# Kernel optimization log

Hardware: AMD Instinct MI355X
Metric: run time of the kernel (lower is better)

## Reference

```python
import jax, jax.numpy as jnp
import numpy as np

N_NODES = 50000
N_EDGES = 800000
D_FEAT = 64      # input_size
D_OUT = 64       # output_size
N_REL = 8
N_BASES = 4


def setup_inputs() -> dict:
    key = jax.random.key(0)
    k1, k2, k3, k4, k5, k6 = jax.random.split(key, 6)
    x = jax.random.normal(k1, (N_NODES, D_FEAT, N_REL), dtype=jnp.float32)
    edge_src = jax.random.randint(k2, (N_EDGES,), 0, N_NODES, dtype=jnp.int32)
    edge_dst = jax.random.randint(k3, (N_EDGES,), 0, N_NODES, dtype=jnp.int32)
    edge_weight = jax.random.uniform(k4, (N_EDGES,), dtype=jnp.float32)
    # basis-decomposed relation weights (xavier-like scale)
    w_bases = jax.random.normal(k5, (N_BASES, D_FEAT, D_OUT), dtype=jnp.float32) * (2.0 / (D_FEAT + D_OUT)) ** 0.5
    w_rel = jax.random.normal(k6, (N_REL, N_BASES), dtype=jnp.float32) * (2.0 / (N_REL + N_BASES)) ** 0.5
    return {"x": x, "edge_src": edge_src, "edge_dst": edge_dst,
            "edge_weight": edge_weight, "w_bases": w_bases, "w_rel": w_rel}


def reference(x, edge_src, edge_dst, edge_weight, w_bases, w_rel):
    # w[r] = sum_b w_rel[r,b] * w_bases[b]  -> [R, d_in, d_out]
    w = jnp.einsum('rb,bio->rio', w_rel, w_bases)
    n_rel = x.shape[-1]
    n_nodes = x.shape[0]
    # sparse adjacency message passing per relation: support_r = A @ x[:, :, r]
    # A @ y == segment_sum over edges (dst <- weight * y[src])
    supports = []
    for r in range(n_rel):  # small fixed relation count
        msgs = edge_weight[:, None] * x[edge_src, :, r]          # [E, d_in]
        agg = jax.ops.segment_sum(msgs, edge_dst, num_segments=n_nodes)  # [N, d_in]
        supports.append(agg)
    tmp = jnp.concatenate(supports, axis=1)                      # [N, R*d_in]
    weights = w.reshape(n_rel * x.shape[1], w.shape[2])          # [R*d_in, d_out]
    out = tmp @ weights                                          # [N, d_out]
    return out
```

## Files before the change

kernel.cpp:

```cpp
#include <hip/hip_runtime.h>
#include <hip/hip_bf16.h>

#define DFEAT   64
#define NREL    8
#define KDIM    512
#define DOUT    64
#define NBASES  4

typedef short short8 __attribute__((ext_vector_type(8)));
typedef float f32x4  __attribute__((ext_vector_type(4)));
typedef unsigned short ushort8 __attribute__((ext_vector_type(8)));

__device__ __forceinline__ unsigned short f2bf(float f) {
    unsigned u = __float_as_uint(f);
    u += 0x7fff + ((u >> 16) & 1);
    return (unsigned short)(u >> 16);
}
__device__ __forceinline__ float bf2f(unsigned short b) {
    return __uint_as_float(((unsigned)b) << 16);
}

__global__ __launch_bounds__(256) void weight_kernel(
    const float* __restrict__ w_rel,
    const float* __restrict__ w_bases,
    unsigned short* __restrict__ wT,
    int* __restrict__ cnt, int n_nodes)
{
    int idx = blockIdx.x * 256 + threadIdx.x;
    int k = idx & 511;
    int o = idx >> 9;
    int i = k >> 3;
    int r = k & 7;
    float s = 0.f;
#pragma unroll
    for (int b = 0; b < NBASES; ++b)
        s += w_rel[r * NBASES + b] * w_bases[(b * DFEAT + i) * DOUT + o];
    wT[o * KDIM + k] = f2bf(s);

    for (int j = idx; j < n_nodes; j += KDIM * DOUT)
        cnt[j] = 0;
}

__global__ __launch_bounds__(256) void fused_kernel(
    const float* __restrict__ x,
    const unsigned short* __restrict__ wT,
    unsigned short* __restrict__ y,
    int n_nodes,
    const int* __restrict__ esrc, const int* __restrict__ edst,
    const float* __restrict__ ew,
    int* __restrict__ cnt, unsigned* __restrict__ bucket,
    int n_edges, int cap, int t_blocks)
{
    const int tid = threadIdx.x;

    if (blockIdx.x >= t_blocks) {
        int e = (blockIdx.x - t_blocks) * 256 + tid;
        if (e < n_edges) {
            int d = edst[e];
            int pos = atomicAdd(&cnt[d], 1);
            if (pos < cap) {
                bucket[(size_t)d * cap + pos] =
                    (unsigned)(esrc[e] & 0xFFFF) | ((unsigned)f2bf(ew[e]) << 16);
            }
        }
        return;
    }

    __shared__ unsigned short ylds[4][16][64];

    const int wid  = tid >> 6;
    const int lane = tid & 63;
    const int quad = lane >> 4;
    const int fi   = lane & 15;

    const int node0 = (blockIdx.x * 4 + wid) * 16;
    int myrow = node0 + fi;
    if (myrow >= n_nodes) myrow = n_nodes - 1;
    const float* xg = x + (size_t)myrow * KDIM + quad * 8;
    const unsigned short* wg = wT + fi * KDIM + quad * 8;

    f32x4 acc0 = {0.f, 0.f, 0.f, 0.f};
    f32x4 acc1 = {0.f, 0.f, 0.f, 0.f};
    f32x4 acc2 = {0.f, 0.f, 0.f, 0.f};
    f32x4 acc3 = {0.f, 0.f, 0.f, 0.f};

#pragma unroll 4
    for (int kb = 0; kb < KDIM; kb += 32) {
        float4 xa = *(const float4*)(xg + kb);
        float4 xb = *(const float4*)(xg + kb + 4);
        short8 a;
        a[0] = f2bf(xa.x); a[1] = f2bf(xa.y); a[2] = f2bf(xa.z); a[3] = f2bf(xa.w);
        a[4] = f2bf(xb.x); a[5] = f2bf(xb.y); a[6] = f2bf(xb.z); a[7] = f2bf(xb.w);

        short8 b0 = *(const short8*)(wg + kb);
        short8 b1 = *(const short8*)(wg + 16 * KDIM + kb);
        short8 b2 = *(const short8*)(wg + 32 * KDIM + kb);
        short8 b3 = *(const short8*)(wg + 48 * KDIM + kb);

        acc0 = __builtin_amdgcn_mfma_f32_16x16x32_bf16(a, b0, acc0, 0, 0, 0);
        acc1 = __builtin_amdgcn_mfma_f32_16x16x32_bf16(a, b1, acc1, 0, 0, 0);
        acc2 = __builtin_amdgcn_mfma_f32_16x16x32_bf16(a, b2, acc2, 0, 0, 0);
        acc3 = __builtin_amdgcn_mfma_f32_16x16x32_bf16(a, b3, acc3, 0, 0, 0);
    }

#pragma unroll
    for (int r = 0; r < 4; ++r) {
        int n = quad * 4 + r;
        ylds[wid][n][fi]      = f2bf(acc0[r]);
        ylds[wid][n][16 + fi] = f2bf(acc1[r]);
        ylds[wid][n][32 + fi] = f2bf(acc2[r]);
        ylds[wid][n][48 + fi] = f2bf(acc3[r]);
    }
    __syncthreads();

    int nl = lane >> 2;
    int cg = (lane & 3) * 16;
    int node = node0 + nl;
    if (node < n_nodes) {
        ushort8 v0 = *(const ushort8*)&ylds[wid][nl][cg];
        ushort8 v1 = *(const ushort8*)&ylds[wid][nl][cg + 8];
        unsigned short* yr = y + (size_t)node * DOUT + cg;
        *(ushort8*)yr       = v0;
        *(ushort8*)(yr + 8) = v1;
    }
}

__global__ __launch_bounds__(256) void gather_kernel(
    const int* __restrict__ cnt, const unsigned* __restrict__ bucket,
    const unsigned short* __restrict__ y,
    float* __restrict__ out, int n_nodes, int cap)
{
    int node = blockIdx.x * 4 + (threadIdx.x >> 6);
    int lane = threadIdx.x & 63;
    int sub = lane >> 3;
    int fi  = lane & 7;
    if (node >= n_nodes) return;

    int deg = cnt[node];
    if (deg > cap) deg = cap;

    unsigned entry = 0;
    if (lane < deg) entry = bucket[(size_t)node * cap + lane];

    float acc[8];
#pragma unroll
    for (int j = 0; j < 8; ++j) acc[j] = 0.f;

    for (int c = 0; c < deg; c += 16) {
        unsigned p0 = __shfl((int)entry, c + sub);
        unsigned p1 = __shfl((int)entry, c + 8 + sub);
        float w0 = __uint_as_float(p0 & 0xFFFF0000u);
        float w1 = __uint_as_float(p1 & 0xFFFF0000u);
        ushort8 y0 = *(const ushort8*)(y + (size_t)(p0 & 0xFFFFu) * DOUT + fi * 8);
        ushort8 y1 = *(const ushort8*)(y + (size_t)(p1 & 0xFFFFu) * DOUT + fi * 8);
#pragma unroll
        for (int j = 0; j < 8; ++j) {
            acc[j] += w0 * bf2f(y0[j]);
            acc[j] += w1 * bf2f(y1[j]);
        }
    }

#pragma unroll
    for (int mask = 8; mask <= 32; mask <<= 1)
#pragma unroll
        for (int j = 0; j < 8; ++j)
            acc[j] += __shfl_xor(acc[j], mask);

    if (sub == 0) {
        float* orow = out + (size_t)node * DOUT + fi * 8;
        *(float4*)orow       = make_float4(acc[0], acc[1], acc[2], acc[3]);
        *(float4*)(orow + 4) = make_float4(acc[4], acc[5], acc[6], acc[7]);
    }
}

extern "C" void kernel_launch(void* const* d_in, const int* in_sizes, int n_in,
                              void* d_out, int out_size, void* d_ws, size_t ws_size,
                              hipStream_t stream) {
    const float* x       = (const float*)d_in[0];
    const int*   esrc    = (const int*)d_in[1];
    const int*   edst    = (const int*)d_in[2];
    const float* ew      = (const float*)d_in[3];
    const float* w_bases = (const float*)d_in[4];
    const float* w_rel   = (const float*)d_in[5];
    float* out = (float*)d_out;

    const int n_nodes = in_sizes[0] / KDIM;
    const int n_edges = in_sizes[1];

    size_t base_words = (size_t)n_nodes * 32 + 16384 + n_nodes;
    int cap = 64;
    while (cap > 16 && (base_words + (size_t)n_nodes * cap) * 4 > ws_size)
        cap -= 16;

    unsigned short* y   = (unsigned short*)d_ws;
    unsigned short* wT  = y + (size_t)n_nodes * DOUT;
    int*      cnt       = (int*)(wT + KDIM * DOUT);
    unsigned* bucket    = (unsigned*)(cnt + n_nodes);

    weight_kernel<<<(KDIM * DOUT) / 256, 256, 0, stream>>>(
        w_rel, w_bases, wT, cnt, n_nodes);

    const int t_blocks = (n_nodes + 63) / 64;
    const int p_blocks = (n_edges + 255) / 256;
    fused_kernel<<<t_blocks + p_blocks, 256, 0, stream>>>(
        x, wT, y, n_nodes,
        esrc, edst, ew, cnt, bucket, n_edges, cap, t_blocks);

    int gblocks = (n_nodes + 3) / 4;
    gather_kernel<<<gblocks, 256, 0, stream>>>(cnt, bucket, y, out, n_nodes, cap);
}
```

Measured before the change: 230.4 us.

## Two-level binning of edges by destination chunk before bucket scatter

Edge placement changes from one global atomic per edge into a per-node bucket to a two-stage scheme. Each block first bins 2048 edges into shared memory by destination chunk and appends them to per-chunk slabs. A new scatter kernel then places each chunk's records using shared-memory counters over a node sub-range. The aim is to localize the random global atomics and bucket writes so they hit L2/MCs with better locality, and the gather is reordered chunk-major to match. The cost is an extra kernel launch, slab traffic, and each scatter block rereading its whole chunk slab (SB-fold redundant reads).

```diff
diff --git a/kernel.cpp b/kernel.cpp
--- a/kernel.cpp
+++ b/kernel.cpp
@@ -7,6 +7,11 @@
 #define DOUT    64
 #define NBASES  4
 
+#define NCHUNK  8
+#define EPB     2048
+#define CAPB    352
+#define SB      8
+
 typedef short short8 __attribute__((ext_vector_type(8)));
 typedef float f32x4  __attribute__((ext_vector_type(4)));
 typedef unsigned short ushort8 __attribute__((ext_vector_type(8)));
@@ -24,7 +29,7 @@
     const float* __restrict__ w_rel,
     const float* __restrict__ w_bases,
     unsigned short* __restrict__ wT,
-    int* __restrict__ cnt, int n_nodes)
+    int* __restrict__ cnt, int* __restrict__ cursor, int n_nodes)
 {
     int idx = blockIdx.x * 256 + threadIdx.x;
     int k = idx & 511;
@@ -37,9 +42,20 @@
         s += w_rel[r * NBASES + b] * w_bases[(b * DFEAT + i) * DOUT + o];
     wT[o * KDIM + k] = f2bf(s);
 
+    if (idx < 16) cursor[idx] = 0;
     for (int j = idx; j < n_nodes; j += KDIM * DOUT)
         cnt[j] = 0;
 }
+
+union SharedK2 {
+    unsigned short ylds[4][16][64];
+    struct {
+        uint2 bin[NCHUNK][CAPB];
+        int bcnt[NCHUNK];
+        int bful[NCHUNK];
+        int bbase[NCHUNK];
+    } b;
+};
 
 __global__ __launch_bounds__(256) void fused_kernel(
     const float* __restrict__ x,
@@ -48,25 +64,61 @@
     int n_nodes,
     const int* __restrict__ esrc, const int* __restrict__ edst,
     const float* __restrict__ ew,
-    int* __restrict__ cnt, unsigned* __restrict__ bucket,
-    int n_edges, int cap, int t_blocks)
+    int* __restrict__ cnt, int* __restrict__ cursor,
+    unsigned* __restrict__ bucket, uint2* __restrict__ slab,
+    int n_edges, int cap, int slab_cap, int chsz, int t_blocks)
 {
     const int tid = threadIdx.x;
+    __shared__ SharedK2 sh;
 
     if (blockIdx.x >= t_blocks) {
-        int e = (blockIdx.x - t_blocks) * 256 + tid;
-        if (e < n_edges) {
-            int d = edst[e];
-            int pos = atomicAdd(&cnt[d], 1);
-            if (pos < cap) {
-                bucket[(size_t)d * cap + pos] =
-                    (unsigned)(esrc[e] & 0xFFFF) | ((unsigned)f2bf(ew[e]) << 16);
+        auto& B = sh.b;
+        if (tid < NCHUNK) B.bcnt[tid] = 0;
+        __syncthreads();
+
+        int e0 = (blockIdx.x - t_blocks) * EPB + tid;
+#pragma unroll
+        for (int j = 0; j < EPB / 256; ++j) {
+            int e = e0 + j * 256;
+            if (e < n_edges) {
+                int d = edst[e];
+                unsigned entry = (unsigned)(esrc[e] & 0xFFFF)
+                               | ((unsigned)f2bf(ew[e]) << 16);
+                int c = d / chsz;
+                int pos = atomicAdd(&B.bcnt[c], 1);
+                if (pos < CAPB) {
+                    B.bin[c][pos] = make_uint2(entry, (unsigned)d);
+                } else {
+                    int p = atomicAdd(&cnt[d], 1);
+                    if (p < cap) bucket[(size_t)d * cap + p] = entry;
+                }
             }
         }
+        __syncthreads();
+
+        if (tid < NCHUNK) {
+            int n = B.bcnt[tid]; if (n > CAPB) n = CAPB;
+            B.bful[tid] = n;
+            B.bbase[tid] = atomicAdd(&cursor[tid], n);
+        }
+        __syncthreads();
+
+#pragma unroll 1
+        for (int c = 0; c < NCHUNK; ++c) {
+            int n = B.bful[c], bb = B.bbase[c];
+            uint2* sc = slab + (size_t)c * slab_cap;
+            for (int i = tid; i < n; i += 256) {
+                uint2 rec = B.bin[c][i];
+                if (bb + i < slab_cap) {
+                    sc[bb + i] = rec;
+                } else {
+                    int p = atomicAdd(&cnt[(int)rec.y], 1);
+                    if (p < cap) bucket[(size_t)rec.y * cap + p] = rec.x;
+                }
+            }
+        }
         return;
     }
-
-    __shared__ unsigned short ylds[4][16][64];
 
     const int wid  = tid >> 6;
     const int lane = tid & 63;
@@ -106,10 +158,10 @@
 #pragma unroll
     for (int r = 0; r < 4; ++r) {
         int n = quad * 4 + r;
-        ylds[wid][n][fi]      = f2bf(acc0[r]);
-        ylds[wid][n][16 + fi] = f2bf(acc1[r]);
-        ylds[wid][n][32 + fi] = f2bf(acc2[r]);
-        ylds[wid][n][48 + fi] = f2bf(acc3[r]);
+        sh.ylds[wid][n][fi]      = f2bf(acc0[r]);
+        sh.ylds[wid][n][16 + fi] = f2bf(acc1[r]);
+        sh.ylds[wid][n][32 + fi] = f2bf(acc2[r]);
+        sh.ylds[wid][n][48 + fi] = f2bf(acc3[r]);
     }
     __syncthreads();
 
@@ -117,38 +169,74 @@
     int cg = (lane & 3) * 16;
     int node = node0 + nl;
     if (node < n_nodes) {
-        ushort8 v0 = *(const ushort8*)&ylds[wid][nl][cg];
-        ushort8 v1 = *(const ushort8*)&ylds[wid][nl][cg + 8];
+        ushort8 v0 = *(const ushort8*)&sh.ylds[wid][nl][cg];
+        ushort8 v1 = *(const ushort8*)&sh.ylds[wid][nl][cg + 8];
         unsigned short* yr = y + (size_t)node * DOUT + cg;
         *(ushort8*)yr       = v0;
         *(ushort8*)(yr + 8) = v1;
     }
 }
 
+__global__ __launch_bounds__(1024) void scatter_kernel(
+    const uint2* __restrict__ slab, const int* __restrict__ cursor,
+    int* __restrict__ cnt, unsigned* __restrict__ bucket,
+    int n_nodes, int cap, int chsz, int slab_cap)
+{
+    __shared__ int lcnt[1024];
+    const int tid = threadIdx.x;
+    const int c = blockIdx.x & (NCHUNK - 1);
+    const int s = blockIdx.x / NCHUNK;
+    const int srsz  = (chsz + SB - 1) / SB;
+    const int nbase = c * chsz + s * srsz;
+    int nspan = srsz;
+    if (nspan > chsz - s * srsz)  nspan = chsz - s * srsz;
+    if (nspan > n_nodes - nbase)  nspan = n_nodes - nbase;
+    if (nspan < 0) nspan = 0;
+
+    for (int i = tid; i < nspan; i += 1024) lcnt[i] = cnt[nbase + i];
+    __syncthreads();
+
+    int total = cursor[c]; if (total > slab_cap) total = slab_cap;
+    const uint2* sl = slab + (size_t)c * slab_cap;
+    for (int i = tid; i < total; i += 1024) {
+        uint2 rec = sl[i];
+        int rel = (int)rec.y - nbase;
+        if ((unsigned)rel < (unsigned)nspan) {
+            int pos = atomicAdd(&lcnt[rel], 1);
+            if (pos < cap)
+                bucket[(size_t)rec.y * cap + pos] = rec.x;
+        }
+    }
+    __syncthreads();
+    for (int i = tid; i < nspan; i += 1024) cnt[nbase + i] = lcnt[i];
+}
+
 __global__ __launch_bounds__(256) void gather_kernel(
     const int* __restrict__ cnt, const unsigned* __restrict__ bucket,
     const unsigned short* __restrict__ y,
-    float* __restrict__ out, int n_nodes, int cap)
+    float* __restrict__ out, int n_nodes, int cap, int chsz)
 {
-    int node = blockIdx.x * 4 + (threadIdx.x >> 6);
+    const int c = blockIdx.x & (NCHUNK - 1);
+    const int q = blockIdx.x / NCHUNK;
+    int rel  = q * 4 + (threadIdx.x >> 6);
+    int node = c * chsz + rel;
     int lane = threadIdx.x & 63;
     int sub = lane >> 3;
     int fi  = lane & 7;
-    if (node >= n_nodes) return;
+    if (rel >= chsz || node >= n_nodes) return;
 
     int deg = cnt[node];
+    unsigned entry = (lane < cap) ? bucket[(size_t)node * cap + lane] : 0u;
     if (deg > cap) deg = cap;
-
-    unsigned entry = 0;
-    if (lane < deg) entry = bucket[(size_t)node * cap + lane];
+    if (lane >= deg) entry = 0;
 
     float acc[8];
 #pragma unroll
     for (int j = 0; j < 8; ++j) acc[j] = 0.f;
 
-    for (int c = 0; c < deg; c += 16) {
-        unsigned p0 = __shfl((int)entry, c + sub);
-        unsigned p1 = __shfl((int)entry, c + 8 + sub);
+    for (int cc = 0; cc < deg; cc += 16) {
+        unsigned p0 = __shfl((int)entry, cc + sub);
+        unsigned p1 = __shfl((int)entry, cc + 8 + sub);
         float w0 = __uint_as_float(p0 & 0xFFFF0000u);
         float w1 = __uint_as_float(p1 & 0xFFFF0000u);
         ushort8 y0 = *(const ushort8*)(y + (size_t)(p0 & 0xFFFFu) * DOUT + fi * 8);
@@ -186,26 +274,39 @@
 
     const int n_nodes = in_sizes[0] / KDIM;
     const int n_edges = in_sizes[1];
-
-    size_t base_words = (size_t)n_nodes * 32 + 16384 + n_nodes;
+    const int chsz = (n_nodes + NCHUNK - 1) / NCHUNK;
+
+    size_t wsw = ws_size / 4;
+    size_t base_words = (size_t)n_nodes * 32 + 16384 + n_nodes + 16;
     int cap = 64;
-    while (cap > 16 && (base_words + (size_t)n_nodes * cap) * 4 > ws_size)
+    while (cap > 16 && base_words + (size_t)n_nodes * cap > wsw)
         cap -= 16;
+    size_t used = base_words + (size_t)n_nodes * cap;
+    size_t rem = (wsw > used) ? (wsw - used) : 0;
+    size_t sc = rem / 16;
+    int slab_cap = (int)(sc > 131072 ? 131072 : sc);
 
     unsigned short* y   = (unsigned short*)d_ws;
     unsigned short* wT  = y + (size_t)n_nodes * DOUT;
     int*      cnt       = (int*)(wT + KDIM * DOUT);
-    unsigned* bucket    = (unsigned*)(cnt + n_nodes);
+    int*      cursor    = cnt + n_nodes;
+    unsigned* bucket    = (unsigned*)(cursor + 16);
+    uint2*    slab      = (uint2*)(bucket + (size_t)n_nodes * cap);
 
     weight_kernel<<<(KDIM * DOUT) / 256, 256, 0, stream>>>(
-        w_rel, w_bases, wT, cnt, n_nodes);
+        w_rel, w_bases, wT, cnt, cursor, n_nodes);
 
     const int t_blocks = (n_nodes + 63) / 64;
-    const int p_blocks = (n_edges + 255) / 256;
+    const int p_blocks = (n_edges + EPB - 1) / EPB;
     fused_kernel<<<t_blocks + p_blocks, 256, 0, stream>>>(
         x, wT, y, n_nodes,
-        esrc, edst, ew, cnt, bucket, n_edges, cap, t_blocks);
-
-    int gblocks = (n_nodes + 3) / 4;
-    gather_kernel<<<gblocks, 256, 0, stream>>>(cnt, bucket, y, out, n_nodes, cap);
-}
+        esrc, edst, ew, cnt, cursor, bucket, slab,
+        n_edges, cap, slab_cap, chsz, t_blocks);
+
+    scatter_kernel<<<NCHUNK * SB, 1024, 0, stream>>>(
+        slab, cursor, cnt, bucket, n_nodes, cap, chsz, slab_cap);
+
+    const int gblocks = NCHUNK * ((chsz + 3) / 4);
+    gather_kernel<<<gblocks, 256, 0, stream>>>(
+        cnt, bucket, y, out, n_nodes, cap, chsz);
+}
```

Result: slower. 246.7 us (+7.1%).

## Replace per-node buckets with coarse chunk binning and LDS-atomic aggregation

Applied to the files above, without the earlier changes.

Edges are now binned into 256 destination-node chunks. Each block stages them in shared-memory bins, then flushes them to per-chunk slabs with an overflow list, instead of doing one global atomic per node. The gather kernel becomes an aggregate kernel. Each 1024-thread block owns a span of 196 nodes, scans its chunk's slab, and accumulates weighted y rows into shared memory with float atomics. The change removes the per-node global atomics and the fixed per-node degree cap, which could drop edges. In exchange, every sub-block rescans the whole chunk slab and pays heavy shared-memory atomic contention.

```diff
diff --git a/kernel.cpp b/kernel.cpp
--- a/kernel.cpp
+++ b/kernel.cpp
@@ -7,6 +7,11 @@
 #define DOUT    64
 #define NBASES  4
 
+#define NC      256
+#define EPB     2048
+#define CAPB    12
+#define SPAN    196
+
 typedef short short8 __attribute__((ext_vector_type(8)));
 typedef float f32x4  __attribute__((ext_vector_type(4)));
 typedef unsigned short ushort8 __attribute__((ext_vector_type(8)));
@@ -24,7 +29,7 @@
     const float* __restrict__ w_rel,
     const float* __restrict__ w_bases,
     unsigned short* __restrict__ wT,
-    int* __restrict__ cnt, int n_nodes)
+    int* __restrict__ cursor)
 {
     int idx = blockIdx.x * 256 + threadIdx.x;
     int k = idx & 511;
@@ -37,9 +42,16 @@
         s += w_rel[r * NBASES + b] * w_bases[(b * DFEAT + i) * DOUT + o];
     wT[o * KDIM + k] = f2bf(s);
 
-    for (int j = idx; j < n_nodes; j += KDIM * DOUT)
-        cnt[j] = 0;
-}
+    if (idx < NC + 8) cursor[idx] = 0;
+}
+
+union SharedK2 {
+    unsigned short ylds[4][16][64];
+    struct {
+        uint2 bin[NC][CAPB];
+        int bcnt[NC];
+    } b;
+};
 
 __global__ __launch_bounds__(256) void fused_kernel(
     const float* __restrict__ x,
@@ -48,25 +60,56 @@
     int n_nodes,
     const int* __restrict__ esrc, const int* __restrict__ edst,
     const float* __restrict__ ew,
-    int* __restrict__ cnt, unsigned* __restrict__ bucket,
-    int n_edges, int cap, int t_blocks)
+    int* __restrict__ cursor,
+    uint2* __restrict__ slab, uint2* __restrict__ ovf,
+    int n_edges, int chsz, int slab_cap, int ovf_cap, int t_blocks)
 {
     const int tid = threadIdx.x;
+    __shared__ SharedK2 sh;
 
     if (blockIdx.x >= t_blocks) {
-        int e = (blockIdx.x - t_blocks) * 256 + tid;
-        if (e < n_edges) {
-            int d = edst[e];
-            int pos = atomicAdd(&cnt[d], 1);
-            if (pos < cap) {
-                bucket[(size_t)d * cap + pos] =
-                    (unsigned)(esrc[e] & 0xFFFF) | ((unsigned)f2bf(ew[e]) << 16);
+        auto& B = sh.b;
+        B.bcnt[tid] = 0;
+        __syncthreads();
+
+        int e0 = (blockIdx.x - t_blocks) * EPB + tid;
+#pragma unroll
+        for (int j = 0; j < EPB / 256; ++j) {
+            int e = e0 + j * 256;
+            if (e < n_edges) {
+                int d = edst[e];
+                unsigned entry = (unsigned)(esrc[e] & 0xFFFF)
+                               | ((unsigned)f2bf(ew[e]) << 16);
+                int c = d / chsz;
+                uint2 rec = make_uint2(entry, (unsigned)d);
+                int pos = atomicAdd(&B.bcnt[c], 1);
+                if (pos < CAPB) {
+                    B.bin[c][pos] = rec;
+                } else {
+                    int p = atomicAdd(&cursor[c], 1);
+                    if (p < slab_cap) slab[(size_t)c * slab_cap + p] = rec;
+                    else { int q = atomicAdd(&cursor[NC], 1);
+                           if (q < ovf_cap) ovf[q] = rec; }
+                }
             }
         }
+        __syncthreads();
+
+        {
+            int c = tid;
+            int n = B.bcnt[c]; if (n > CAPB) n = CAPB;
+            int bb = atomicAdd(&cursor[c], n);
+            uint2* sc = slab + (size_t)c * slab_cap;
+            for (int i = 0; i < n; ++i) {
+                uint2 rec = B.bin[c][i];
+                int p = bb + i;
+                if (p < slab_cap) sc[p] = rec;
+                else { int q = atomicAdd(&cursor[NC], 1);
+                       if (q < ovf_cap) ovf[q] = rec; }
+            }
+        }
         return;
     }
-
-    __shared__ unsigned short ylds[4][16][64];
 
     const int wid  = tid >> 6;
     const int lane = tid & 63;
@@ -106,10 +149,10 @@
 #pragma unroll
     for (int r = 0; r < 4; ++r) {
         int n = quad * 4 + r;
-        ylds[wid][n][fi]      = f2bf(acc0[r]);
-        ylds[wid][n][16 + fi] = f2bf(acc1[r]);
-        ylds[wid][n][32 + fi] = f2bf(acc2[r]);
-        ylds[wid][n][48 + fi] = f2bf(acc3[r]);
+        sh.ylds[wid][n][fi]      = f2bf(acc0[r]);
+        sh.ylds[wid][n][16 + fi] = f2bf(acc1[r]);
+        sh.ylds[wid][n][32 + fi] = f2bf(acc2[r]);
+        sh.ylds[wid][n][48 + fi] = f2bf(acc3[r]);
     }
     __syncthreads();
 
@@ -117,60 +160,72 @@
     int cg = (lane & 3) * 16;
     int node = node0 + nl;
     if (node < n_nodes) {
-        ushort8 v0 = *(const ushort8*)&ylds[wid][nl][cg];
-        ushort8 v1 = *(const ushort8*)&ylds[wid][nl][cg + 8];
+        ushort8 v0 = *(const ushort8*)&sh.ylds[wid][nl][cg];
+        ushort8 v1 = *(const ushort8*)&sh.ylds[wid][nl][cg + 8];
         unsigned short* yr = y + (size_t)node * DOUT + cg;
         *(ushort8*)yr       = v0;
         *(ushort8*)(yr + 8) = v1;
     }
 }
 
-__global__ __launch_bounds__(256) void gather_kernel(
-    const int* __restrict__ cnt, const unsigned* __restrict__ bucket,
+__global__ __launch_bounds__(1024) void aggregate_kernel(
+    const uint2* __restrict__ slab, const uint2* __restrict__ ovf,
+    const int* __restrict__ cursor,
     const unsigned short* __restrict__ y,
-    float* __restrict__ out, int n_nodes, int cap)
+    float* __restrict__ out, int n_nodes, int chsz, int nsub,
+    int slab_cap, int ovf_cap)
 {
-    int node = blockIdx.x * 4 + (threadIdx.x >> 6);
-    int lane = threadIdx.x & 63;
-    int sub = lane >> 3;
-    int fi  = lane & 7;
-    if (node >= n_nodes) return;
-
-    int deg = cnt[node];
-    if (deg > cap) deg = cap;
-
-    unsigned entry = 0;
-    if (lane < deg) entry = bucket[(size_t)node * cap + lane];
-
-    float acc[8];
-#pragma unroll
-    for (int j = 0; j < 8; ++j) acc[j] = 0.f;
-
-    for (int c = 0; c < deg; c += 16) {
-        unsigned p0 = __shfl((int)entry, c + sub);
-        unsigned p1 = __shfl((int)entry, c + 8 + sub);
-        float w0 = __uint_as_float(p0 & 0xFFFF0000u);
-        float w1 = __uint_as_float(p1 & 0xFFFF0000u);
-        ushort8 y0 = *(const ushort8*)(y + (size_t)(p0 & 0xFFFFu) * DOUT + fi * 8);
-        ushort8 y1 = *(const ushort8*)(y + (size_t)(p1 & 0xFFFFu) * DOUT + fi * 8);
-#pragma unroll
-        for (int j = 0; j < 8; ++j) {
-            acc[j] += w0 * bf2f(y0[j]);
-            acc[j] += w1 * bf2f(y1[j]);
-        }
-    }
-
-#pragma unroll
-    for (int mask = 8; mask <= 32; mask <<= 1)
-#pragma unroll
-        for (int j = 0; j < 8; ++j)
-            acc[j] += __shfl_xor(acc[j], mask);
-
-    if (sub == 0) {
-        float* orow = out + (size_t)node * DOUT + fi * 8;
-        *(float4*)orow       = make_float4(acc[0], acc[1], acc[2], acc[3]);
-        *(float4*)(orow + 4) = make_float4(acc[4], acc[5], acc[6], acc[7]);
-    }
+    __shared__ float acc[SPAN * DOUT];
+    const int tid = threadIdx.x;
+    const int c = blockIdx.x / nsub;
+    const int s = blockIdx.x % nsub;
+    const int nbase = c * chsz + s * SPAN;
+    int nspan = SPAN;
+    if (nspan > chsz - s * SPAN)  nspan = chsz - s * SPAN;
+    if (nspan > n_nodes - nbase)  nspan = n_nodes - nbase;
+    if (nspan <= 0) return;
+
+    for (int i = tid; i < nspan * DOUT; i += 1024) acc[i] = 0.f;
+    __syncthreads();
+
+    const int lane = tid & 63;
+    const int wv   = tid >> 6;
+    int total = cursor[c]; if (total > slab_cap) total = slab_cap;
+    const uint2* sl = slab + (size_t)c * slab_cap;
+    int per  = (total + 15) >> 4;
+    int rbeg = wv * per;
+    int rend = rbeg + per; if (rend > total) rend = total;
+    const unsigned short* yl = y + lane;
+
+#pragma unroll 4
+    for (int i = rbeg; i < rend; ++i) {
+        uint2 rec = sl[i];
+        int rel = (int)rec.y - nbase;
+        if ((unsigned)rel < (unsigned)nspan) {
+            float w = __uint_as_float(rec.x & 0xFFFF0000u);
+            int src = (int)(rec.x & 0xFFFFu);
+            atomicAdd(&acc[rel * DOUT + lane],
+                      w * bf2f(yl[(size_t)src * DOUT]));
+        }
+    }
+
+    int novf = cursor[NC]; if (novf > ovf_cap) novf = ovf_cap;
+    for (int i = tid; i < novf; i += 1024) {
+        uint2 rec = ovf[i];
+        int rel = (int)rec.y - nbase;
+        if ((unsigned)rel < (unsigned)nspan) {
+            float w = __uint_as_float(rec.x & 0xFFFF0000u);
+            int src = (int)(rec.x & 0xFFFFu);
+            for (int j = 0; j < DOUT; ++j)
+                atomicAdd(&acc[rel * DOUT + j],
+                          w * bf2f(y[(size_t)src * DOUT + j]));
+        }
+    }
+    __syncthreads();
+
+    float4* o4 = (float4*)(out + (size_t)nbase * DOUT);
+    const float4* a4 = (const float4*)acc;
+    for (int i = tid; i < nspan * (DOUT / 4); i += 1024) o4[i] = a4[i];
 }
 
 extern "C" void kernel_launch(void* const* d_in, const int* in_sizes, int n_in,
@@ -186,26 +241,35 @@
 
     const int n_nodes = in_sizes[0] / KDIM;
     const int n_edges = in_sizes[1];
-
-    size_t base_words = (size_t)n_nodes * 32 + 16384 + n_nodes;
-    int cap = 64;
-    while (cap > 16 && (base_words + (size_t)n_nodes * cap) * 4 > ws_size)
-        cap -= 16;
+    const int chsz = (n_nodes + NC - 1) / NC;
+    const int nsub = (chsz + SPAN - 1) / SPAN;
+
+    size_t wsw = ws_size / 4;
+    size_t base = (size_t)n_nodes * 32 + 16384 + 264;
+    size_t avail = (wsw > base) ? wsw - base : 0;
+    size_t slab_budget = avail * 7 / 8;
+    int slab_cap = (int)(slab_budget / (2 * NC));
+    if (slab_cap > 4096) slab_cap = 4096;
+    size_t ovf_words = avail - (size_t)2 * NC * slab_cap;
+    size_t oc = ovf_words / 2;
+    int ovf_cap = (int)(oc > (size_t)n_edges ? (size_t)n_edges : oc);
 
     unsigned short* y   = (unsigned short*)d_ws;
     unsigned short* wT  = y + (size_t)n_nodes * DOUT;
-    int*      cnt       = (int*)(wT + KDIM * DOUT);
-    unsigned* bucket    = (unsigned*)(cnt + n_nodes);
+    int*   cursor       = (int*)(wT + KDIM * DOUT);
+    uint2* slab         = (uint2*)(cursor + 264);
+    uint2* ovf          = slab + (size_t)NC * slab_cap;
 
     weight_kernel<<<(KDIM * DOUT) / 256, 256, 0, stream>>>(
-        w_rel, w_bases, wT, cnt, n_nodes);
+        w_rel, w_bases, wT, cursor);
 
     const int t_blocks = (n_nodes + 63) / 64;
-    const int p_blocks = (n_edges + 255) / 256;
+    const int p_blocks = (n_edges + EPB - 1) / EPB;
     fused_kernel<<<t_blocks + p_blocks, 256, 0, stream>>>(
         x, wT, y, n_nodes,
-        esrc, edst, ew, cnt, bucket, n_edges, cap, t_blocks);
-
-    int gblocks = (n_nodes + 3) / 4;
-    gather_kernel<<<gblocks, 256, 0, stream>>>(cnt, bucket, y, out, n_nodes, cap);
-}
+        esrc, edst, ew, cursor, slab, ovf,
+        n_edges, chsz, slab_cap, ovf_cap, t_blocks);
+
+    aggregate_kernel<<<NC * nsub, 1024, 0, stream>>>(
+        slab, ovf, cursor, y, out, n_nodes, chsz, nsub, slab_cap, ovf_cap);
+}
```

New measurement: 476.7 us. +106.9%, slower.
